# Optimization experiments

Measured on AMD Instinct MI355X. Metric: run time of the kernel, lower is better.

Reference implementation:

```python
import jax, jax.numpy as jnp
import numpy as np

CEP_ORDER = 24
ALPHA = 0.42
BETA = 0.2
ONSET = 2
IR_LENGTH = 128


def _freqt_matrix(in_order, out_order, alpha):
    # diffsptk FrequencyTransform precomputed matrix A (L2, L1): c2 = c1 @ A.T
    L1, L2 = in_order + 1, out_order + 1
    A = np.zeros((L2, L1), dtype=np.float64)
    A[0, :] = alpha ** np.arange(L1)
    if L2 > 1 and L1 > 1:
        A[1, 1:] = (alpha ** np.arange(L1 - 1, dtype=np.float64)) * np.arange(1, L1) * (1.0 - alpha * alpha)
    for i in range(2, L2):
        for j in range(1, L1):
            A[i, j] = A[i - 1, j - 1] + alpha * (A[i, j - 1] - A[i - 1, j])
    return A


def _mc2b_matrix(M, alpha):
    # b[m] = mc[m] - alpha*b[m+1]  =>  b[m] = sum_{j>=m} (-alpha)^(j-m) mc[j]
    j = np.arange(M + 1)
    P = j[None, :] - j[:, None]
    return np.where(P >= 0, (-alpha) ** np.maximum(P, 0), 0.0)


def _b2mc_matrix(M, alpha):
    # mc[m] = b[m] + alpha*b[m+1]
    return np.eye(M + 1) + alpha * np.eye(M + 1, k=1)


# constants derived from hyperparameters (buffers in the torch module)
A_FT = jnp.asarray(_freqt_matrix(CEP_ORDER, IR_LENGTH - 1, -ALPHA), dtype=jnp.float32)   # (128, 25)
A_MC2B = jnp.asarray(_mc2b_matrix(CEP_ORDER, ALPHA), dtype=jnp.float32)                  # (25, 25)
A_B2MC = jnp.asarray(_b2mc_matrix(CEP_ORDER, ALPHA), dtype=jnp.float32)                  # (25, 25)
_w = np.full(CEP_ORDER + 1, 1.0 + BETA, dtype=np.float32)
_w[:ONSET] = 1.0
WEIGHT = jnp.asarray(_w)                                                                  # (25,)


def _mc2en(mc):
    # mel-cepstrum -> energy: warp to linear cepstrum (len 128), power spectrum, r[0]
    c = jnp.einsum('...m,lm->...l', mc, A_FT)                 # (..., 128)
    spec = jnp.exp(2.0 * jnp.fft.rfft(c, n=IR_LENGTH).real)   # (..., 65), real power spectrum
    # r[0] of irfft(spec): DC + Nyquist once, interior bins twice (IR_LENGTH even)
    r0 = (spec[..., 0] + spec[..., -1] + 2.0 * jnp.sum(spec[..., 1:-1], axis=-1)) / IR_LENGTH
    return r0                                                  # (...,)


def setup_inputs() -> dict:
    key = jax.random.key(0)
    mc = 0.2 * jax.random.normal(key, (16, 32768, CEP_ORDER + 1), dtype=jnp.float32)
    return {"mc": mc}


def reference(mc):
    e1 = _mc2en(mc)                                            # energy before postfilter
    mc2 = mc * WEIGHT                                          # intensity-weighted cepstrum
    e2 = _mc2en(mc2)                                           # energy after weighting
    b2 = jnp.einsum('...m,nm->...n', mc2, A_MC2B)              # mc -> MLSA coefficients
    b2 = b2.at[..., 0].add(0.5 * jnp.log(e1 / e2))             # energy compensation on b[0]
    return jnp.einsum('...m,nm->...n', b2, A_B2MC)             # MLSA -> mel-cepstrum
```

## Files before the change

kernel.cpp:

```cpp
#include <hip/hip_runtime.h>


namespace cg {

constexpr int L  = 128;
constexpr int M1 = 25;

struct CosTab { double v[L]; };
constexpr CosTab make_costab() {
    CosTab t{};
    const double PI = 3.14159265358979323846;
    for (int i = 0; i < L; ++i) {
        int j = (i <= 64) ? i : i - 128;
        double x = (2.0 * PI * (double)j) / 128.0;
        double x2 = x * x, term = 1.0, s = 1.0;
        for (int n = 1; n <= 16; ++n) {
            term *= -x2 / ((2.0 * n - 1.0) * (2.0 * n));
            s += term;
        }
        t.v[i] = s;
    }
    return t;
}
constexpr CosTab CT = make_costab();

struct AMat { double v[L][M1]; };
constexpr AMat make_aft() {
    AMat A{};
    const double al = -0.42;
    double p = 1.0;
    for (int j = 0; j < M1; ++j) { A.v[0][j] = p; p *= al; }
    double q = 1.0;
    for (int j = 1; j < M1; ++j) { A.v[1][j] = q * (double)j * (1.0 - al * al); q *= al; }
    for (int i = 2; i < L; ++i)
        for (int j = 1; j < M1; ++j)
            A.v[i][j] = A.v[i - 1][j - 1] + al * (A.v[i][j - 1] - A.v[i - 1][j]);
    return A;
}
constexpr AMat AFT = make_aft();

struct Chunk { double v[8][M1]; };
template <int K0>
constexpr Chunk make_chunk() {
    Chunk c{};
    for (int kk = 0; kk < 8; ++kk) {
        int k = K0 + kk;
        for (int m = 0; m < M1; ++m) {
            double s = 0.0;
            for (int l = 0; l < L; ++l)
                s += AFT.v[l][m] * CT.v[(k * l) & 127];
            c.v[kk][m] = s;
        }
    }
    return c;
}
constexpr Chunk CH0 = make_chunk<0>();
constexpr Chunk CH1 = make_chunk<8>();
constexpr Chunk CH2 = make_chunk<16>();
constexpr Chunk CH3 = make_chunk<24>();
constexpr Chunk CH4 = make_chunk<32>();
constexpr Chunk CH5 = make_chunk<40>();
constexpr Chunk CH6 = make_chunk<48>();
constexpr Chunk CH7 = make_chunk<56>();
constexpr Chunk CH8 = make_chunk<64>();

constexpr double chunkval(int bin, int m) {
    const Chunk* chs[9] = { &CH0, &CH1, &CH2, &CH3, &CH4, &CH5, &CH6, &CH7, &CH8 };
    return chs[bin >> 3]->v[bin & 7][m];
}

constexpr double blogical(int k, int col) {
    const double LOG2E = 1.44269504088896340736;
    if (col >= 130) return (k == 25) ? -1.0e4 : 0.0;
    int bin = (col < 65) ? col : (col - 65);
    if (k == 25) return (bin == 0 || bin == 64) ? 0.0 : 1.0;
    if (k > 25) return 0.0;
    double c = LOG2E * 2.0 * chunkval(bin, k);
    if (col >= 65 && k >= 2) c *= 1.2;
    return c;
}

constexpr unsigned short f2h(double v) {
    if (v == 0.0) return 0;
    unsigned short s = 0;
    if (v < 0) { s = 0x8000; v = -v; }
    int e = 0;
    while (v >= 2.0) { v *= 0.5; ++e; }
    while (v < 1.0)  { v *= 2.0; --e; }
    if (e > 15) return (unsigned short)(s | 0x7c00);
    if (e < -14) return s;
    int mant = (int)((v - 1.0) * 1024.0 + 0.5);
    if (mant == 1024) { mant = 0; ++e; if (e > 15) return (unsigned short)(s | 0x7c00); }
    return (unsigned short)(s | ((e + 15) << 10) | mant);
}

struct Tile { unsigned short v[64][8]; };
template <int N>
constexpr Tile make_tile() {
    Tile t{};
    for (int l = 0; l < 64; ++l)
        for (int j = 0; j < 8; ++j)
            t.v[l][j] = f2h(blogical((l >> 4) * 8 + j, N * 16 + (l & 15)));
    return t;
}
constexpr Tile T0 = make_tile<0>();
constexpr Tile T1 = make_tile<1>();
constexpr Tile T2 = make_tile<2>();
constexpr Tile T3 = make_tile<3>();
constexpr Tile T4 = make_tile<4>();
constexpr Tile T5 = make_tile<5>();
constexpr Tile T6 = make_tile<6>();
constexpr Tile T7 = make_tile<7>();
constexpr Tile T8 = make_tile<8>();

struct BH { alignas(16) unsigned short v[9][64][8]; };
constexpr BH make_bh() {
    BH b{};
    const Tile* ts[9] = { &T0, &T1, &T2, &T3, &T4, &T5, &T6, &T7, &T8 };
    for (int n = 0; n < 9; ++n)
        for (int l = 0; l < 64; ++l)
            for (int j = 0; j < 8; ++j)
                b.v[n][l][j] = ts[n]->v[l][j];
    return b;
}

}

__device__ const cg::BH g_Bh = cg::make_bh();

typedef _Float16 f16x8 __attribute__((ext_vector_type(8)));
typedef float    f32x4 __attribute__((ext_vector_type(4)));

__global__ __launch_bounds__(256, 5)
void mcpf_kernel(const float* __restrict__ mc, float* __restrict__ out) {
    __shared__ __align__(16) float sbuf[256 * 25 + 8];
    __shared__ float d_lds[272];
    const int tid = threadIdx.x;
    const long long base = (long long)blockIdx.x * (256LL * 25);

    const int lane = tid & 63;
    const int wv   = tid >> 6;
    const int r0   = lane & 15;
    const int kg   = lane >> 4;

    f16x8 bfrag[9];
#pragma unroll
    for (int n = 0; n < 9; ++n)
        bfrag[n] = *reinterpret_cast<const f16x8*>(&g_Bh.v[n][lane][0]);

    const float4* __restrict__ src4 = reinterpret_cast<const float4*>(mc + base);
    float4* sb4 = reinterpret_cast<float4*>(sbuf);
    float4 rowreg[7];
#pragma unroll
    for (int i = 0; i < 7; ++i) {
        int idx = tid + i * 256;
        if (idx < 1600) {
            rowreg[i] = src4[idx];
            sb4[idx]  = rowreg[i];
        }
    }
    __syncthreads();

#pragma unroll
    for (int g = 0; g < 4; ++g) {
        const int rowbase = wv * 64 + g * 16;
        const float* __restrict__ arow = &sbuf[(rowbase + r0) * 25 + kg * 8];

        float tmp[8];
#pragma unroll
        for (int j = 0; j < 8; ++j) tmp[j] = arow[j];
        f16x8 af;
        af[0] = (_Float16)tmp[0];
        af[1] = (kg == 3) ? (_Float16)1.0f : (_Float16)tmp[1];
#pragma unroll
        for (int j = 2; j < 8; ++j)
            af[j] = (kg == 3) ? (_Float16)0.0f : (_Float16)tmp[j];

        float s1 = 0.0f, s2 = 0.0f;
#pragma unroll
        for (int n = 0; n < 9; ++n) {
            f32x4 acc = {0.f, 0.f, 0.f, 0.f};
            acc = __builtin_amdgcn_mfma_f32_16x16x32_f16(bfrag[n], af, acc, 0, 0, 0);
            float e0 = __builtin_amdgcn_exp2f(acc[0]);
            float e1 = __builtin_amdgcn_exp2f(acc[1]);
            float e2 = __builtin_amdgcn_exp2f(acc[2]);
            float e3 = __builtin_amdgcn_exp2f(acc[3]);
            if (n < 4) {
                s1 += (e0 + e1) + (e2 + e3);
            } else if (n == 4) {
                float h = (e0 + e1) + (e2 + e3);
                bool c = (kg == 0);
                s1 += c ? e0 : 0.0f;
                s2 += c ? (h - e0) : h;
            } else {
                s2 += (e0 + e1) + (e2 + e3);
            }
        }

        s1 += __shfl_xor(s1, 16);
        s1 += __shfl_xor(s1, 32);
        s2 += __shfl_xor(s2, 16);
        s2 += __shfl_xor(s2, 32);

        if (kg == 0) {
            float d = 0.34657359027997264f *
                      (__builtin_amdgcn_logf(s1) - __builtin_amdgcn_logf(s2));
            d_lds[rowbase + r0] = d;
        }
    }

    __syncthreads();

    float4* __restrict__ dst4 = reinterpret_cast<float4*>(out + base);
#pragma unroll
    for (int i = 0; i < 7; ++i) {
        int idx = tid + i * 256;
        if (idx < 1600) {
            float4 v = rowreg[i];
            int f = idx * 4;
            int q = f / 25;
            int r = f - 25 * q;
            float dv0 = d_lds[q];
            float dv1 = d_lds[q + 1];
            v.x *= (r     < 2)                  ? 1.0f : 1.2f;
            v.y *= (r + 1 < 2 || r + 1 == 25)   ? 1.0f : 1.2f;
            v.z *= (r + 2 == 25 || r + 2 == 26) ? 1.0f : 1.2f;
            v.w *= (r + 3 == 25 || r + 3 == 26) ? 1.0f : 1.2f;
            if (r == 0)  v.x += dv0;
            if (r == 22) v.w += dv1;
            if (r == 23) v.z += dv1;
            if (r == 24) v.y += dv1;
            dst4[idx] = v;
        }
    }
}

extern "C" void kernel_launch(void* const* d_in, const int* in_sizes, int n_in,
                              void* d_out, int out_size, void* d_ws, size_t ws_size,
                              hipStream_t stream) {
    const float* mc = (const float*)d_in[0];
    float* out = (float*)d_out;
    const int rows = in_sizes[0] / 25;
    const int blocks = rows / 256;
    mcpf_kernel<<<dim3(blocks), dim3(256), 0, stream>>>(mc, out);
}
```

Baseline: 26.17 us.

## Give each wavefront a private LDS slice and drop block-wide barriers

Each wavefront now loads its own 64 rows into a private shared-memory region, computes their energy corrections, and writes its own output. This replaces the two block-level __syncthreads with s_waitcnt on LDS, and reloads the row data from LDS instead of holding it in registers. The register saving and the changed occupancy hint (5 to 6 blocks) aim for more waves in flight. The risk is that within-wave LDS visibility relies on waitcnt ordering rather than a formal barrier.

```diff
diff --git a/kernel.cpp b/kernel.cpp
--- a/kernel.cpp
+++ b/kernel.cpp
@@ -131,40 +131,41 @@
 typedef _Float16 f16x8 __attribute__((ext_vector_type(8)));
 typedef float    f32x4 __attribute__((ext_vector_type(4)));
 
-__global__ __launch_bounds__(256, 5)
+constexpr int WCHUNK = 1672;
+
+__global__ __launch_bounds__(256, 6)
 void mcpf_kernel(const float* __restrict__ mc, float* __restrict__ out) {
-    __shared__ __align__(16) float sbuf[256 * 25 + 8];
-    __shared__ float d_lds[272];
-    const int tid = threadIdx.x;
-    const long long base = (long long)blockIdx.x * (256LL * 25);
-
+    __shared__ __align__(16) float sbuf[4 * WCHUNK];
+    const int tid  = threadIdx.x;
     const int lane = tid & 63;
     const int wv   = tid >> 6;
     const int r0   = lane & 15;
     const int kg   = lane >> 4;
 
+    float* __restrict__ wbuf = &sbuf[wv * WCHUNK];
+    float* __restrict__ dreg = wbuf + 1600;
+
+    const long long base4 = (long long)blockIdx.x * 1600 + wv * 400;
+
     f16x8 bfrag[9];
 #pragma unroll
     for (int n = 0; n < 9; ++n)
         bfrag[n] = *reinterpret_cast<const f16x8*>(&g_Bh.v[n][lane][0]);
 
-    const float4* __restrict__ src4 = reinterpret_cast<const float4*>(mc + base);
-    float4* sb4 = reinterpret_cast<float4*>(sbuf);
-    float4 rowreg[7];
-#pragma unroll
-    for (int i = 0; i < 7; ++i) {
-        int idx = tid + i * 256;
-        if (idx < 1600) {
-            rowreg[i] = src4[idx];
-            sb4[idx]  = rowreg[i];
-        }
-    }
-    __syncthreads();
+    const float4* __restrict__ src4 =
+        reinterpret_cast<const float4*>(mc) + base4;
+    float4* wb4 = reinterpret_cast<float4*>(wbuf);
+#pragma unroll
+    for (int j = 0; j < 7; ++j) {
+        int idx = lane + j * 64;
+        if (idx < 400) wb4[idx] = src4[idx];
+    }
+    asm volatile("s_waitcnt lgkmcnt(0)" ::: "memory");
 
 #pragma unroll
     for (int g = 0; g < 4; ++g) {
-        const int rowbase = wv * 64 + g * 16;
-        const float* __restrict__ arow = &sbuf[(rowbase + r0) * 25 + kg * 8];
+        const int rowbase = g * 16;
+        const float* __restrict__ arow = &wbuf[(rowbase + r0) * 25 + kg * 8];
 
         float tmp[8];
 #pragma unroll
@@ -205,23 +206,23 @@
         if (kg == 0) {
             float d = 0.34657359027997264f *
                       (__builtin_amdgcn_logf(s1) - __builtin_amdgcn_logf(s2));
-            d_lds[rowbase + r0] = d;
-        }
-    }
-
-    __syncthreads();
-
-    float4* __restrict__ dst4 = reinterpret_cast<float4*>(out + base);
-#pragma unroll
-    for (int i = 0; i < 7; ++i) {
-        int idx = tid + i * 256;
-        if (idx < 1600) {
-            float4 v = rowreg[i];
+            dreg[rowbase + r0] = d;
+        }
+    }
+
+    asm volatile("s_waitcnt lgkmcnt(0)" ::: "memory");
+
+    float4* __restrict__ dst4 = reinterpret_cast<float4*>(out) + base4;
+#pragma unroll
+    for (int j = 0; j < 7; ++j) {
+        int idx = lane + j * 64;
+        if (idx < 400) {
+            float4 v = wb4[idx];
             int f = idx * 4;
             int q = f / 25;
             int r = f - 25 * q;
-            float dv0 = d_lds[q];
-            float dv1 = d_lds[q + 1];
+            float dv0 = dreg[q];
+            float dv1 = dreg[q + 1];
             v.x *= (r     < 2)                  ? 1.0f : 1.2f;
             v.y *= (r + 1 < 2 || r + 1 == 25)   ? 1.0f : 1.2f;
             v.z *= (r + 2 == 25 || r + 2 == 26) ? 1.0f : 1.2f;
```

Result: faster. 24.54 us (-6.2%).
